# Performance work log

Measured on AMD Instinct MI355X. Metric: run time of the kernel, lower is better.

The kernel has to match this reference:

```python
import jax, jax.numpy as jnp
import numpy as np

N_NODES = 100000
N_EDGES = 200000
N_GRAPHS = 4096
NODE_DIM = 256
OUT_DIM = 768
LAYERS = 4
NODE_FEATS = 9
EDGE_FEATS = 3
NODE_VOCAB = 119  # max categorical size across node features (padded)
EDGE_VOCAB = 22   # max categorical size across edge features (padded)


def setup_inputs() -> dict:
    key = jax.random.key(0)
    ks = jax.random.split(key, 16)
    x_cat = jax.random.randint(ks[0], (N_NODES, NODE_FEATS), 0, 2)
    edge_attr = jax.random.randint(ks[1], (N_EDGES, EDGE_FEATS), 0, 2)
    edge_index = jax.random.randint(ks[2], (2, N_EDGES), 0, N_NODES)
    batch = jnp.sort(jax.random.randint(ks[3], (N_NODES,), 0, N_GRAPHS))
    s = 0.02
    node_emb = jax.random.normal(ks[4], (NODE_FEATS, NODE_VOCAB, NODE_DIM), jnp.float32) * s
    edge_emb = jax.random.normal(ks[5], (EDGE_FEATS, EDGE_VOCAB, NODE_DIM), jnp.float32) * s
    W1 = jax.random.normal(ks[6], (LAYERS, NODE_DIM, 2 * NODE_DIM), jnp.float32) * s
    b1 = jnp.zeros((LAYERS, 2 * NODE_DIM), jnp.float32)
    W2 = jax.random.normal(ks[7], (LAYERS, 2 * NODE_DIM, NODE_DIM), jnp.float32) * s
    b2 = jnp.zeros((LAYERS, NODE_DIM), jnp.float32)
    pW1 = jax.random.normal(ks[8], (NODE_DIM, NODE_DIM), jnp.float32) * s
    pb1 = jnp.zeros((NODE_DIM,), jnp.float32)
    pW2 = jax.random.normal(ks[9], (NODE_DIM, OUT_DIM), jnp.float32) * s
    pb2 = jnp.zeros((OUT_DIM,), jnp.float32)
    return {
        "x_cat": x_cat, "edge_attr": edge_attr, "edge_index": edge_index, "batch": batch,
        "node_emb": node_emb, "edge_emb": edge_emb,
        "W1": W1, "b1": b1, "W2": W2, "b2": b2,
        "pW1": pW1, "pb1": pb1, "pW2": pW2, "pb2": pb2,
    }


def _encode(tables, idx):
    # tables: [F, V, D], idx: [N, F] -> sum over features of embedding lookups -> [N, D]
    return jnp.sum(jax.vmap(lambda tbl, i: tbl[i], in_axes=(0, 1))(tables, idx), axis=0)


def reference(x_cat, edge_attr, edge_index, batch, node_emb, edge_emb,
              W1, b1, W2, b2, pW1, pb1, pW2, pb2):
    x = _encode(node_emb, x_cat)          # [N, D]
    e = _encode(edge_emb, edge_attr)      # [E, D]
    src, dst = edge_index[0], edge_index[1]
    for l in range(LAYERS):
        # GINEConv: aggr = sum_{j in N(i)} relu(x_j + e_ij); out = mlp((1+eps)*x_i + aggr), eps=0
        msg = jax.nn.relu(x[src] + e)                                  # [E, D]
        agg = jax.ops.segment_sum(msg, dst, num_segments=N_NODES)     # [N, D]
        h = x + agg
        h = jax.nn.relu(h @ W1[l] + b1[l]) @ W2[l] + b2[l]
        x = jax.nn.relu(h)
    g = jax.ops.segment_sum(x, batch, num_segments=N_GRAPHS)          # [G, D]
    g = jax.nn.relu(g @ pW1 + pb1) @ pW2 + pb2                         # [G, OUT]
    norm = jnp.maximum(jnp.linalg.norm(g, axis=-1, keepdims=True), 1e-12)
    return g / norm
```

## Files before the change

### kernel.cpp

```cpp
#include <hip/hip_runtime.h>

#define N_NODES 100000
#define N_NODES_PAD 100032
#define N_EDGES 200000
#define N_GRAPHS 4096
#define D 256
#define D2 512
#define OUTD 768
#define LAYERS 4
#define NODE_FEATS 9
#define EDGE_FEATS 3
#define NODE_VOCAB 119
#define EDGE_VOCAB 22
#define BM 64
#define GB 8

typedef __attribute__((ext_vector_type(8))) short bf16x8;
typedef __attribute__((ext_vector_type(4))) float f32x4;
typedef unsigned short ushort_t;
typedef unsigned int uint_t;

__device__ __forceinline__ ushort_t f2b(float f) {
    union { float f; uint_t u; } x; x.f = f;
    uint_t r = (x.u + 0x7FFFu + ((x.u >> 16) & 1u)) >> 16;
    return (ushort_t)r;
}
__device__ __forceinline__ float b2f(ushort_t u) {
    union { uint_t u; float f; } x; x.u = ((uint_t)u) << 16;
    return x.f;
}

__device__ __forceinline__ int lower_bound_i(const int* a, int n, int v) {
    int lo = 0, hi = n;
    while (lo < hi) { int mid = (lo + hi) >> 1; if (a[mid] < v) lo = mid + 1; else hi = mid; }
    return lo;
}

__global__ __launch_bounds__(256) void encode_nodes_k(const int* __restrict__ xcat,
                                                      const float* __restrict__ tab,
                                                      ushort_t* __restrict__ X) {
    int n = blockIdx.x, d = threadIdx.x;
    float acc = 0.f;
#pragma unroll
    for (int f = 0; f < NODE_FEATS; ++f) {
        int idx = xcat[n * NODE_FEATS + f];
        acc += tab[((size_t)f * NODE_VOCAB + idx) * D + d];
    }
    X[(size_t)n * D + d] = f2b(acc);
}

__global__ __launch_bounds__(256) void count_k(const int* __restrict__ eidx, int* deg) {
    int e = blockIdx.x * 256 + threadIdx.x;
    if (e < N_EDGES) atomicAdd(&deg[eidx[N_EDGES + e]], 1);
}

#define SCAN_B 1024
__global__ __launch_bounds__(256) void scan1_k(const int* __restrict__ deg,
                                               int* __restrict__ excl, int* __restrict__ bsum) {
    __shared__ int sh[256];
    int b = blockIdx.x, t = threadIdx.x;
    int base = b * SCAN_B + t * 4;
    int d0 = (base + 0) < N_NODES ? deg[base + 0] : 0;
    int d1 = (base + 1) < N_NODES ? deg[base + 1] : 0;
    int d2 = (base + 2) < N_NODES ? deg[base + 2] : 0;
    int d3 = (base + 3) < N_NODES ? deg[base + 3] : 0;
    int s = d0 + d1 + d2 + d3;
    sh[t] = s; __syncthreads();
    for (int off = 1; off < 256; off <<= 1) {
        int x = (t >= off) ? sh[t - off] : 0;
        __syncthreads();
        sh[t] += x;
        __syncthreads();
    }
    int incl = sh[t];
    int ex = incl - s;
    if (base + 0 < N_NODES) excl[base + 0] = ex;
    if (base + 1 < N_NODES) excl[base + 1] = ex + d0;
    if (base + 2 < N_NODES) excl[base + 2] = ex + d0 + d1;
    if (base + 3 < N_NODES) excl[base + 3] = ex + d0 + d1 + d2;
    if (t == 255) bsum[b] = incl;
}

__global__ void scan2_k(int* bsum, int nb) {
    __shared__ int sh[128];
    int t = threadIdx.x;
    int v = (t < nb) ? bsum[t] : 0;
    sh[t] = v; __syncthreads();
    for (int off = 1; off < 128; off <<= 1) {
        int x = (t >= off) ? sh[t - off] : 0;
        __syncthreads();
        sh[t] += x;
        __syncthreads();
    }
    if (t < nb) bsum[t] = sh[t] - v;
}

__global__ __launch_bounds__(256) void scan3_k(int* __restrict__ offs, int* __restrict__ cursor,
                                               const int* __restrict__ bsum) {
    int i = blockIdx.x * 256 + threadIdx.x;
    if (i < N_NODES) {
        int v = offs[i] + bsum[i >> 10];
        offs[i] = v;
        cursor[i] = v;
    }
}

__global__ __launch_bounds__(256) void fill_k(const int* __restrict__ eidx,
                                              const int* __restrict__ eattr,
                                              int* cursor, int2* __restrict__ elist) {
    int e = blockIdx.x * 256 + threadIdx.x;
    if (e < N_EDGES) {
        int src = eidx[e];
        int dst = eidx[N_EDGES + e];
        int pa = eattr[e * EDGE_FEATS + 0] | (eattr[e * EDGE_FEATS + 1] << 8)
               | (eattr[e * EDGE_FEATS + 2] << 16);
        int pos = atomicAdd(&cursor[dst], 1);
        elist[pos] = make_int2(src, pa);
    }
}

__global__ __launch_bounds__(256) void gather_k(const ushort4* __restrict__ X4,
                                                const float4* __restrict__ eemb4,
                                                const int* __restrict__ offs,
                                                const int* __restrict__ deg,
                                                const int2* __restrict__ elist,
                                                ushort4* __restrict__ H4) {
    int n = blockIdx.x * 4 + (threadIdx.x >> 6);
    int lane = threadIdx.x & 63;
    int start = offs[n], dg = deg[n];
    ushort4 xv = X4[(size_t)n * 64 + lane];
    float acc[4] = {b2f(xv.x), b2f(xv.y), b2f(xv.z), b2f(xv.w)};
    if (dg > 0) {
        int2 sp = elist[start];
        ushort4 sv = X4[(size_t)sp.x * 64 + lane];
        for (int i = 0; i < dg; ++i) {
            int2 spn = sp; ushort4 svn = sv;
            if (i + 1 < dg) {
                spn = elist[start + i + 1];
                svn = X4[(size_t)spn.x * 64 + lane];
            }
            float4 t0 = eemb4[(size_t)((sp.y      ) & 255) * 64 + lane];
            float4 t1 = eemb4[((size_t)EDGE_VOCAB + ((sp.y >> 8) & 255)) * 64 + lane];
            float4 t2 = eemb4[((size_t)2 * EDGE_VOCAB + ((sp.y >> 16) & 255)) * 64 + lane];
            acc[0] += fmaxf(b2f(sv.x) + t0.x + t1.x + t2.x, 0.f);
            acc[1] += fmaxf(b2f(sv.y) + t0.y + t1.y + t2.y, 0.f);
            acc[2] += fmaxf(b2f(sv.z) + t0.z + t1.z + t2.z, 0.f);
            acc[3] += fmaxf(b2f(sv.w) + t0.w + t1.w + t2.w, 0.f);
            sp = spn; sv = svn;
        }
    }
    ushort4 hv;
    hv.x = f2b(acc[0]); hv.y = f2b(acc[1]); hv.z = f2b(acc[2]); hv.w = f2b(acc[3]);
    H4[(size_t)n * 64 + lane] = hv;
}

__global__ __launch_bounds__(256) void pack1_k(const float* __restrict__ W1, ushort_t* __restrict__ apack) {
    size_t i = (size_t)blockIdx.x * 256 + threadIdx.x;
    int l = (int)(i >> 14);
    int rem = (int)(i & 16383);
    int ntg = rem >> 9;
    int rem2 = rem & 511;
    int kk = rem2 >> 6;
    int lane = rem2 & 63;
    int n = ntg * 16 + (lane & 15);
    int k0 = kk * 32 + (lane >> 4) * 8;
    const float* w = W1 + ((size_t)l * D + k0) * D2 + n;
    ushort_t* o = apack + i * 8;
#pragma unroll
    for (int j = 0; j < 8; ++j) o[j] = f2b(w[(size_t)j * D2]);
}

__global__ __launch_bounds__(256) void pack2_k(const float* __restrict__ W2, ushort_t* __restrict__ bpack) {
    size_t i = (size_t)blockIdx.x * 256 + threadIdx.x;
    int l = (int)(i >> 14);
    int rem = (int)(i & 16383);
    int ntg = rem >> 10;
    int rem2 = rem & 1023;
    int kk = rem2 >> 6;
    int lane = rem2 & 63;
    int n = ntg * 16 + (lane & 15);
    int k0 = kk * 32 + (lane >> 4) * 8;
    const float* w = W2 + ((size_t)l * D2 + k0) * D + n;
    ushort_t* o = bpack + i * 8;
#pragma unroll
    for (int j = 0; j < 8; ++j) o[j] = f2b(w[(size_t)j * D]);
}

__global__ __launch_bounds__(512, 4) void mlp_k(const ushort_t* __restrict__ H,
                                                const ushort_t* __restrict__ apack,
                                                const float* __restrict__ b1,
                                                const ushort_t* __restrict__ bpack,
                                                const float* __restrict__ b2,
                                                ushort_t* __restrict__ X) {
    __shared__ __align__(16) char hA[BM * 512];
    __shared__ __align__(16) char midh[BM * 512];
    const int t = threadIdx.x;
    const int wid = t >> 6, lane = t & 63;
    const int l15 = lane & 15, g = lane >> 4;
    const size_t r0 = (size_t)blockIdx.x * BM;

    {
        const char* src = (const char*)(H + r0 * D);
#pragma unroll
        for (int c = 0; c < 4; ++c) {
            int Lb = (c * 512 + t) * 16;
            int row = Lb >> 9;
            int Sb = Lb ^ ((row & 7) << 4);
            *(uint4*)(hA + Sb) = *(const uint4*)(src + Lb);
        }
    }

    f32x4 acc2[2][4];
#pragma unroll
    for (int a = 0; a < 2; ++a)
#pragma unroll
        for (int b = 0; b < 4; ++b) { f32x4 z = {0.f,0.f,0.f,0.f}; acc2[a][b] = z; }

    bf16x8 AfA[2], AfB[2], WfA[2], WfB[2];
#pragma unroll
    for (int nt = 0; nt < 2; ++nt)
        AfA[nt] = *(const bf16x8*)(apack + ((size_t)((0 * 16 + wid * 2 + nt) * 8 + 0) * 64 + lane) * 8);

    __syncthreads();

#pragma unroll
    for (int half = 0; half < 2; ++half) {
        f32x4 acc1[2][4];
#pragma unroll
        for (int a = 0; a < 2; ++a)
#pragma unroll
            for (int b = 0; b < 4; ++b) { f32x4 z = {0.f,0.f,0.f,0.f}; acc1[a][b] = z; }

#pragma unroll
        for (int kk = 0; kk < 8; ++kk) {
            bf16x8 Bf[4];
#pragma unroll
            for (int mt = 0; mt < 4; ++mt) {
                int m = mt * 16 + l15;
                Bf[mt] = *(const bf16x8*)(hA + ((m * 512 + (kk * 32 + g * 8) * 2) ^ ((m & 7) << 4)));
            }
            bf16x8* cur = (kk & 1) ? AfB : AfA;
            bf16x8* nxt = (kk & 1) ? AfA : AfB;
            if (kk < 7) {
#pragma unroll
                for (int nt = 0; nt < 2; ++nt)
                    nxt[nt] = *(const bf16x8*)(apack +
                        ((size_t)((half * 16 + wid * 2 + nt) * 8 + kk + 1) * 64 + lane) * 8);
            }
            __builtin_amdgcn_s_setprio(1);
#pragma unroll
            for (int nt = 0; nt < 2; ++nt)
#pragma unroll
                for (int mt = 0; mt < 4; ++mt)
                    acc1[nt][mt] = __builtin_amdgcn_mfma_f32_16x16x32_bf16(cur[nt], Bf[mt], acc1[nt][mt], 0, 0, 0);
            __builtin_amdgcn_s_setprio(0);
        }

#pragma unroll
        for (int nt = 0; nt < 2; ++nt)
            WfA[nt] = *(const bf16x8*)(bpack +
                ((size_t)((wid * 2 + nt) * 16 + half * 8 + 0) * 64 + lane) * 8);

#pragma unroll
        for (int nt = 0; nt < 2; ++nt) {
            int n0l = (wid * 2 + nt) * 16 + g * 4;
            f32x4 bv = *(const f32x4*)(b1 + half * 256 + n0l);
#pragma unroll
            for (int mt = 0; mt < 4; ++mt) {
                int m = mt * 16 + l15;
                ushort_t us[4];
#pragma unroll
                for (int r = 0; r < 4; ++r)
                    us[r] = f2b(fmaxf(acc1[nt][mt][r] + bv[r], 0.f));
                uint2 pk;
                pk.x = (uint_t)us[0] | ((uint_t)us[1] << 16);
                pk.y = (uint_t)us[2] | ((uint_t)us[3] << 16);
                *(uint2*)(midh + ((m * 512 + n0l * 2) ^ ((m & 7) << 4))) = pk;
            }
        }
        __syncthreads();

#pragma unroll
        for (int kk = 0; kk < 8; ++kk) {
            bf16x8 Mf[4];
#pragma unroll
            for (int mt = 0; mt < 4; ++mt) {
                int m = mt * 16 + l15;
                Mf[mt] = *(const bf16x8*)(midh + ((m * 512 + (kk * 32 + g * 8) * 2) ^ ((m & 7) << 4)));
            }
            bf16x8* cur = (kk & 1) ? WfB : WfA;
            bf16x8* nxt = (kk & 1) ? WfA : WfB;
            if (kk < 7) {
#pragma unroll
                for (int nt = 0; nt < 2; ++nt)
                    nxt[nt] = *(const bf16x8*)(bpack +
                        ((size_t)((wid * 2 + nt) * 16 + half * 8 + kk + 1) * 64 + lane) * 8);
            }
            __builtin_amdgcn_s_setprio(1);
#pragma unroll
            for (int nt = 0; nt < 2; ++nt)
#pragma unroll
                for (int mt = 0; mt < 4; ++mt)
                    acc2[nt][mt] = __builtin_amdgcn_mfma_f32_16x16x32_bf16(cur[nt], Mf[mt], acc2[nt][mt], 0, 0, 0);
            __builtin_amdgcn_s_setprio(0);
        }

        if (half == 0) {
#pragma unroll
            for (int nt = 0; nt < 2; ++nt)
                AfA[nt] = *(const bf16x8*)(apack +
                    ((size_t)((1 * 16 + wid * 2 + nt) * 8 + 0) * 64 + lane) * 8);
        }
        __syncthreads();
    }

#pragma unroll
    for (int nt = 0; nt < 2; ++nt) {
        int n0 = (wid * 2 + nt) * 16 + g * 4;
        f32x4 bv = *(const f32x4*)(b2 + n0);
#pragma unroll
        for (int mt = 0; mt < 4; ++mt) {
            int m = mt * 16 + l15;
            ushort_t us[4];
#pragma unroll
            for (int r = 0; r < 4; ++r)
                us[r] = f2b(fmaxf(acc2[nt][mt][r] + bv[r], 0.f));
            uint2 pk;
            pk.x = (uint_t)us[0] | ((uint_t)us[1] << 16);
            pk.y = (uint_t)us[2] | ((uint_t)us[3] << 16);
            *(uint2*)(X + (r0 + m) * D + n0) = pk;
        }
    }
}

__global__ __launch_bounds__(256) void final_k(const ushort4* __restrict__ X4,
                                               const int* __restrict__ batch,
                                               const float* __restrict__ pW1,
                                               const float* __restrict__ pb1,
                                               const float* __restrict__ pW2,
                                               const float* __restrict__ pb2,
                                               float* __restrict__ out) {
    __shared__ float gin[GB][D];
    __shared__ float mid[GB][D];
    __shared__ float red[GB][256];
    __shared__ int bnd[GB + 1];
    const int g0 = blockIdx.x * GB, t = threadIdx.x;
    const int wid = t >> 6, lane = t & 63;
    if (t <= GB) bnd[t] = lower_bound_i(batch, N_NODES, g0 + t);
    __syncthreads();

#pragma unroll
    for (int qq = 0; qq < 2; ++qq) {
        int q = wid + qq * 4;
        f32x4 a = {0.f, 0.f, 0.f, 0.f};
        for (int n = bnd[q]; n < bnd[q + 1]; ++n) {
            ushort4 v = X4[(size_t)n * 64 + lane];
            a.x += b2f(v.x); a.y += b2f(v.y); a.z += b2f(v.z); a.w += b2f(v.w);
        }
        *(f32x4*)&gin[q][lane * 4] = a;
    }
    __syncthreads();

    {
        float m_[GB];
        float bb = pb1[t];
#pragma unroll
        for (int q = 0; q < GB; ++q) m_[q] = bb;
        for (int k = 0; k < D; ++k) {
            float w = pW1[(size_t)k * D + t];
#pragma unroll
            for (int q = 0; q < GB; ++q) m_[q] += gin[q][k] * w;
        }
#pragma unroll
        for (int q = 0; q < GB; ++q) mid[q][t] = fmaxf(m_[q], 0.f);
    }
    __syncthreads();

    float a0[GB], a1[GB], a2[GB];
    {
        float b0 = pb2[t], b1_ = pb2[t + 256], b2_ = pb2[t + 512];
#pragma unroll
        for (int q = 0; q < GB; ++q) { a0[q] = b0; a1[q] = b1_; a2[q] = b2_; }
        for (int k = 0; k < D; ++k) {
            float w0 = pW2[(size_t)k * OUTD + t];
            float w1 = pW2[(size_t)k * OUTD + 256 + t];
            float w2 = pW2[(size_t)k * OUTD + 512 + t];
#pragma unroll
            for (int q = 0; q < GB; ++q) {
                float mv = mid[q][k];
                a0[q] += mv * w0; a1[q] += mv * w1; a2[q] += mv * w2;
            }
        }
    }
#pragma unroll
    for (int q = 0; q < GB; ++q)
        red[q][t] = a0[q] * a0[q] + a1[q] * a1[q] + a2[q] * a2[q];
    __syncthreads();
    for (int s = 128; s > 0; s >>= 1) {
        if (t < s) {
#pragma unroll
            for (int q = 0; q < GB; ++q) red[q][t] += red[q][t + s];
        }
        __syncthreads();
    }
#pragma unroll
    for (int q = 0; q < GB; ++q) {
        float inv = 1.f / fmaxf(sqrtf(red[q][0]), 1e-12f);
        out[(size_t)(g0 + q) * OUTD + t]       = a0[q] * inv;
        out[(size_t)(g0 + q) * OUTD + 256 + t] = a1[q] * inv;
        out[(size_t)(g0 + q) * OUTD + 512 + t] = a2[q] * inv;
    }
}

extern "C" void kernel_launch(void* const* d_in, const int* in_sizes, int n_in,
                              void* d_out, int out_size, void* d_ws, size_t ws_size,
                              hipStream_t stream) {
    const int*   x_cat      = (const int*)d_in[0];
    const int*   edge_attr  = (const int*)d_in[1];
    const int*   edge_index = (const int*)d_in[2];
    const int*   batch      = (const int*)d_in[3];
    const float* node_emb   = (const float*)d_in[4];
    const float* edge_emb   = (const float*)d_in[5];
    const float* W1  = (const float*)d_in[6];
    const float* b1  = (const float*)d_in[7];
    const float* W2  = (const float*)d_in[8];
    const float* b2  = (const float*)d_in[9];
    const float* pW1 = (const float*)d_in[10];
    const float* pb1 = (const float*)d_in[11];
    const float* pW2 = (const float*)d_in[12];
    const float* pb2 = (const float*)d_in[13];
    float* out = (float*)d_out;

    char* p = (char*)d_ws;
    auto carve = [&](size_t bytes) { char* q = p; p += (bytes + 255) & ~(size_t)255; return q; };
    ushort_t* X      = (ushort_t*)carve((size_t)N_NODES_PAD * D * 2);
    ushort_t* H      = (ushort_t*)carve((size_t)N_NODES_PAD * D * 2);
    int*      deg    = (int*)carve((size_t)N_NODES * 4);
    int*      offs   = (int*)carve((size_t)(N_NODES + 8) * 4);
    int*      cursor = (int*)carve((size_t)(N_NODES + 8) * 4);
    int*      bsum   = (int*)carve(1024);
    int2*     elist  = (int2*)carve((size_t)N_EDGES * 8);
    ushort_t* apack1 = (ushort_t*)carve((size_t)LAYERS * 32 * 8 * 64 * 8 * 2);
    ushort_t* bpack2 = (ushort_t*)carve((size_t)LAYERS * 16 * 16 * 64 * 8 * 2);

    const int NB = (N_NODES + SCAN_B - 1) / SCAN_B;

    pack1_k<<<256, 256, 0, stream>>>(W1, apack1);
    pack2_k<<<256, 256, 0, stream>>>(W2, bpack2);
    hipMemsetAsync(deg, 0, (size_t)N_NODES * 4, stream);
    count_k<<<(N_EDGES + 255) / 256, 256, 0, stream>>>(edge_index, deg);
    scan1_k<<<NB, 256, 0, stream>>>(deg, offs, bsum);
    scan2_k<<<1, 128, 0, stream>>>(bsum, NB);
    scan3_k<<<(N_NODES + 255) / 256, 256, 0, stream>>>(offs, cursor, bsum);
    fill_k<<<(N_EDGES + 255) / 256, 256, 0, stream>>>(edge_index, edge_attr, cursor, elist);

    encode_nodes_k<<<N_NODES, 256, 0, stream>>>(x_cat, node_emb, X);

    for (int l = 0; l < LAYERS; ++l) {
        gather_k<<<N_NODES / 4, 256, 0, stream>>>((const ushort4*)X, (const float4*)edge_emb,
                                                  offs, deg, elist, (ushort4*)H);
        mlp_k<<<(N_NODES_PAD) / BM, 512, 0, stream>>>(
            H,
            apack1 + (size_t)l * 32 * 8 * 64 * 8,
            b1 + (size_t)l * D2,
            bpack2 + (size_t)l * 16 * 16 * 64 * 8,
            b2 + (size_t)l * D,
            X);
    }

    final_k<<<N_GRAPHS / GB, 256, 0, stream>>>((const ushort4*)X, batch, pW1, pb1, pW2, pb2, out);
}
```

Baseline: 713.5 us.

## Fuse edge gather-aggregate into MLP kernel with ping-pong node buffers

Removes the separate gather kernel and performs the GINE neighbor aggregation directly inside the MLP kernel, writing the aggregated rows straight into the shared-memory A tile. This avoids writing and re-reading the H intermediate through global memory and saves one launch per layer. Because the next layer's input can no longer be overwritten in place, X is double-buffered across two workspace arrays. The output store is also staged through shared memory for coalesced 16-byte writes. The trade-off is that each 512-thread block now spends a latency-bound gather phase before its matrix math, with only 8 waves per block to hide the irregular loads.

```diff
diff --git a/kernel.cpp b/kernel.cpp
--- a/kernel.cpp
+++ b/kernel.cpp
@@ -119,41 +119,6 @@
     }
 }
 
-__global__ __launch_bounds__(256) void gather_k(const ushort4* __restrict__ X4,
-                                                const float4* __restrict__ eemb4,
-                                                const int* __restrict__ offs,
-                                                const int* __restrict__ deg,
-                                                const int2* __restrict__ elist,
-                                                ushort4* __restrict__ H4) {
-    int n = blockIdx.x * 4 + (threadIdx.x >> 6);
-    int lane = threadIdx.x & 63;
-    int start = offs[n], dg = deg[n];
-    ushort4 xv = X4[(size_t)n * 64 + lane];
-    float acc[4] = {b2f(xv.x), b2f(xv.y), b2f(xv.z), b2f(xv.w)};
-    if (dg > 0) {
-        int2 sp = elist[start];
-        ushort4 sv = X4[(size_t)sp.x * 64 + lane];
-        for (int i = 0; i < dg; ++i) {
-            int2 spn = sp; ushort4 svn = sv;
-            if (i + 1 < dg) {
-                spn = elist[start + i + 1];
-                svn = X4[(size_t)spn.x * 64 + lane];
-            }
-            float4 t0 = eemb4[(size_t)((sp.y      ) & 255) * 64 + lane];
-            float4 t1 = eemb4[((size_t)EDGE_VOCAB + ((sp.y >> 8) & 255)) * 64 + lane];
-            float4 t2 = eemb4[((size_t)2 * EDGE_VOCAB + ((sp.y >> 16) & 255)) * 64 + lane];
-            acc[0] += fmaxf(b2f(sv.x) + t0.x + t1.x + t2.x, 0.f);
-            acc[1] += fmaxf(b2f(sv.y) + t0.y + t1.y + t2.y, 0.f);
-            acc[2] += fmaxf(b2f(sv.z) + t0.z + t1.z + t2.z, 0.f);
-            acc[3] += fmaxf(b2f(sv.w) + t0.w + t1.w + t2.w, 0.f);
-            sp = spn; sv = svn;
-        }
-    }
-    ushort4 hv;
-    hv.x = f2b(acc[0]); hv.y = f2b(acc[1]); hv.z = f2b(acc[2]); hv.w = f2b(acc[3]);
-    H4[(size_t)n * 64 + lane] = hv;
-}
-
 __global__ __launch_bounds__(256) void pack1_k(const float* __restrict__ W1, ushort_t* __restrict__ apack) {
     size_t i = (size_t)blockIdx.x * 256 + threadIdx.x;
     int l = (int)(i >> 14);
@@ -186,12 +151,16 @@
     for (int j = 0; j < 8; ++j) o[j] = f2b(w[(size_t)j * D]);
 }
 
-__global__ __launch_bounds__(512, 4) void mlp_k(const ushort_t* __restrict__ H,
+__global__ __launch_bounds__(512, 4) void mlp_k(const ushort4* __restrict__ X4in,
+                                                const float4* __restrict__ eemb4,
+                                                const int* __restrict__ offs,
+                                                const int* __restrict__ deg,
+                                                const int2* __restrict__ elist,
                                                 const ushort_t* __restrict__ apack,
                                                 const float* __restrict__ b1,
                                                 const ushort_t* __restrict__ bpack,
                                                 const float* __restrict__ b2,
-                                                ushort_t* __restrict__ X) {
+                                                ushort_t* __restrict__ Xout) {
     __shared__ __align__(16) char hA[BM * 512];
     __shared__ __align__(16) char midh[BM * 512];
     const int t = threadIdx.x;
@@ -199,29 +168,52 @@
     const int l15 = lane & 15, g = lane >> 4;
     const size_t r0 = (size_t)blockIdx.x * BM;
 
-    {
-        const char* src = (const char*)(H + r0 * D);
-#pragma unroll
-        for (int c = 0; c < 4; ++c) {
-            int Lb = (c * 512 + t) * 16;
-            int row = Lb >> 9;
-            int Sb = Lb ^ ((row & 7) << 4);
-            *(uint4*)(hA + Sb) = *(const uint4*)(src + Lb);
-        }
-    }
-
-    f32x4 acc2[2][4];
-#pragma unroll
-    for (int a = 0; a < 2; ++a)
-#pragma unroll
-        for (int b = 0; b < 4; ++b) { f32x4 z = {0.f,0.f,0.f,0.f}; acc2[a][b] = z; }
-
     bf16x8 AfA[2], AfB[2], WfA[2], WfB[2];
 #pragma unroll
     for (int nt = 0; nt < 2; ++nt)
         AfA[nt] = *(const bf16x8*)(apack + ((size_t)((0 * 16 + wid * 2 + nt) * 8 + 0) * 64 + lane) * 8);
 
-    __syncthreads();
+#pragma unroll
+    for (int i = 0; i < 8; ++i) {
+        int row = wid * 8 + i;
+        int n = (int)r0 + row;
+        float acc[4] = {0.f, 0.f, 0.f, 0.f};
+        if (n < N_NODES) {
+            ushort4 xv = X4in[(size_t)n * 64 + lane];
+            acc[0] = b2f(xv.x); acc[1] = b2f(xv.y); acc[2] = b2f(xv.z); acc[3] = b2f(xv.w);
+            int start = offs[n], dg = deg[n];
+            if (dg > 0) {
+                int2 sp = elist[start];
+                ushort4 sv = X4in[(size_t)sp.x * 64 + lane];
+                for (int e = 0; e < dg; ++e) {
+                    int2 spn = sp; ushort4 svn = sv;
+                    if (e + 1 < dg) {
+                        spn = elist[start + e + 1];
+                        svn = X4in[(size_t)spn.x * 64 + lane];
+                    }
+                    float4 t0 = eemb4[(size_t)((sp.y      ) & 255) * 64 + lane];
+                    float4 t1 = eemb4[((size_t)EDGE_VOCAB + ((sp.y >> 8) & 255)) * 64 + lane];
+                    float4 t2 = eemb4[((size_t)2 * EDGE_VOCAB + ((sp.y >> 16) & 255)) * 64 + lane];
+                    acc[0] += fmaxf(b2f(sv.x) + t0.x + t1.x + t2.x, 0.f);
+                    acc[1] += fmaxf(b2f(sv.y) + t0.y + t1.y + t2.y, 0.f);
+                    acc[2] += fmaxf(b2f(sv.z) + t0.z + t1.z + t2.z, 0.f);
+                    acc[3] += fmaxf(b2f(sv.w) + t0.w + t1.w + t2.w, 0.f);
+                    sp = spn; sv = svn;
+                }
+            }
+        }
+        uint2 pk;
+        pk.x = (uint_t)f2b(acc[0]) | ((uint_t)f2b(acc[1]) << 16);
+        pk.y = (uint_t)f2b(acc[2]) | ((uint_t)f2b(acc[3]) << 16);
+        *(uint2*)(hA + ((row * 512 + lane * 8) ^ ((row & 7) << 4))) = pk;
+    }
+    __syncthreads();
+
+    f32x4 acc2[2][4];
+#pragma unroll
+    for (int a = 0; a < 2; ++a)
+#pragma unroll
+        for (int b = 0; b < 4; ++b) { f32x4 z = {0.f,0.f,0.f,0.f}; acc2[a][b] = z; }
 
 #pragma unroll
     for (int half = 0; half < 2; ++half) {
@@ -328,7 +320,18 @@
             uint2 pk;
             pk.x = (uint_t)us[0] | ((uint_t)us[1] << 16);
             pk.y = (uint_t)us[2] | ((uint_t)us[3] << 16);
-            *(uint2*)(X + (r0 + m) * D + n0) = pk;
+            *(uint2*)(midh + ((m * 512 + n0 * 2) ^ ((m & 7) << 4))) = pk;
+        }
+    }
+    __syncthreads();
+    {
+        char* dst = (char*)Xout + r0 * 512;
+#pragma unroll
+        for (int j = 0; j < 4; ++j) {
+            int Lb = t * 64 + j * 16;
+            int row = Lb >> 9;
+            int Sb = Lb ^ ((row & 7) << 4);
+            *(uint4*)(dst + Lb) = *(const uint4*)(midh + Sb);
         }
     }
 }
@@ -433,8 +436,8 @@
 
     char* p = (char*)d_ws;
     auto carve = [&](size_t bytes) { char* q = p; p += (bytes + 255) & ~(size_t)255; return q; };
-    ushort_t* X      = (ushort_t*)carve((size_t)N_NODES_PAD * D * 2);
-    ushort_t* H      = (ushort_t*)carve((size_t)N_NODES_PAD * D * 2);
+    ushort_t* Xa     = (ushort_t*)carve((size_t)N_NODES_PAD * D * 2);
+    ushort_t* Xb     = (ushort_t*)carve((size_t)N_NODES_PAD * D * 2);
     int*      deg    = (int*)carve((size_t)N_NODES * 4);
     int*      offs   = (int*)carve((size_t)(N_NODES + 8) * 4);
     int*      cursor = (int*)carve((size_t)(N_NODES + 8) * 4);
@@ -454,19 +457,20 @@
     scan3_k<<<(N_NODES + 255) / 256, 256, 0, stream>>>(offs, cursor, bsum);
     fill_k<<<(N_EDGES + 255) / 256, 256, 0, stream>>>(edge_index, edge_attr, cursor, elist);
 
-    encode_nodes_k<<<N_NODES, 256, 0, stream>>>(x_cat, node_emb, X);
-
+    encode_nodes_k<<<N_NODES, 256, 0, stream>>>(x_cat, node_emb, Xa);
+
+    ushort_t* xin = Xa;
+    ushort_t* xout = Xb;
     for (int l = 0; l < LAYERS; ++l) {
-        gather_k<<<N_NODES / 4, 256, 0, stream>>>((const ushort4*)X, (const float4*)edge_emb,
-                                                  offs, deg, elist, (ushort4*)H);
-        mlp_k<<<(N_NODES_PAD) / BM, 512, 0, stream>>>(
-            H,
+        mlp_k<<<N_NODES_PAD / BM, 512, 0, stream>>>(
+            (const ushort4*)xin, (const float4*)edge_emb, offs, deg, elist,
             apack1 + (size_t)l * 32 * 8 * 64 * 8,
             b1 + (size_t)l * D2,
             bpack2 + (size_t)l * 16 * 16 * 64 * 8,
             b2 + (size_t)l * D,
-            X);
-    }
-
-    final_k<<<N_GRAPHS / GB, 256, 0, stream>>>((const ushort4*)X, batch, pW1, pb1, pW2, pb2, out);
-}
+            xout);
+        ushort_t* tmp = xin; xin = xout; xout = tmp;
+    }
+
+    final_k<<<N_GRAPHS / GB, 256, 0, stream>>>((const ushort4*)xin, batch, pW1, pb1, pW2, pb2, out);
+}
```

Result: slower. 732.6 us (+2.7%).
